# Kernel optimization log

Measured on AMD Instinct MI355X. Metric: run time of the kernel, lower is better.

## Reference

```python
import jax, jax.numpy as jnp
import numpy as np

D = 50          # half-window
K = 2 * D + 1   # 101 window positions
P_SIZE = 100    # predictive-alignment hidden dim


def setup_inputs() -> dict:
    key = jax.random.key(0)
    ks = jax.random.split(key, 5)
    B, S, CQ, CC = 2, 2048, 256, 256
    q = jax.random.normal(ks[0], (B, S, CQ), jnp.float32)
    c_t = jax.random.normal(ks[1], (B, S, CC), jnp.float32)
    W_a = jax.random.normal(ks[2], (CC, CQ), jnp.float32) / np.sqrt(CQ).astype(np.float32)
    W_p = jax.random.normal(ks[3], (P_SIZE, CC), jnp.float32) / np.sqrt(CC).astype(np.float32)
    V_p = jax.random.normal(ks[4], (1, P_SIZE), jnp.float32) / np.sqrt(P_SIZE).astype(np.float32)
    return {"q": q, "c_t": c_t, "W_a": W_a, "W_p": W_p, "V_p": V_p}


def reference(q, c_t, W_a, W_p, V_p):
    B, S, CQ = q.shape
    # predictive alignment: p in (0, S), one predicted center per (b, s)
    p = S * jax.nn.sigmoid(jnp.tanh(c_t @ W_p.T) @ V_p.T)[..., 0]          # [B,S]
    offs = jnp.arange(-D, D + 1)                                           # [K]
    # torch .long() truncates toward zero (raw can be negative)
    raw = jnp.trunc(p[..., None] + offs[None, None, :] + 1.0).astype(jnp.int32)
    # clamp to [0, S+1] then mod (S+1): index 0 == padded (invalid) row,
    # matching torch's NaN-padded row 0 (S+1 wraps to 0 via the modulo)
    idx = jnp.clip(raw, 0, S + 1) % (S + 1)                                # [B,S,K]
    mask = idx == 0                                                        # invalid window slots
    # pad row 0 (torch pads with NaN then zeroes the NaN rows; we pad with 0
    # and mask by index -> identical math for finite q)
    q_pad = jnp.concatenate([jnp.zeros((B, 1, CQ), q.dtype), q], axis=1)   # [B,S+1,CQ]
    gathered = jnp.take_along_axis(q_pad, idx.reshape(B, S * K, 1), axis=1)
    q1 = jnp.where(mask[..., None], 0.0, gathered.reshape(B, S, K, CQ))    # [B,S,K,CQ]
    # score: W_a projection then dot with context
    Wq = jnp.einsum("bskq,cq->bskc", q1, W_a)                              # [B,S,K,CC]
    a = jnp.einsum("bskc,bsc->bsk", Wq, c_t)                               # [B,S,K]
    a = jnp.where(mask, -jnp.inf, a)
    attn = jax.nn.softmax(a, axis=2)                                       # [B,S,K]
    # gaussian decay centered at floor(p) (p > 0 so trunc == floor)
    exponent = -2.0 * (((offs[None, None, :] + jnp.trunc(p)[..., None] - p[..., None]) / D) ** 2)
    w = attn * jnp.exp(exponent)                                           # [B,S,K]
    s_t = jnp.einsum("bsk,bskc->bsc", w, q1)                               # [B,S,CQ]
    return s_t
```

## Files before the change

### kernel.cpp

```cpp
#include <hip/hip_runtime.h>
#include <math.h>

#define S_LEN 2048
#define NB    2
#define CQ_   256
#define CC_   256
#define DH    50
#define KW    101
#define PS    100
#define RB    4
#define HPAD  128
#define WTH   1e-5f

__global__ __launch_bounds__(128) void k_prep(const float* __restrict__ Wp,
                                              float* __restrict__ WpT) {
  const int c = blockIdx.x, j = threadIdx.x;
  WpT[c * HPAD + j] = (j < PS) ? Wp[j * CC_ + c] : 0.0f;
}

__global__ __launch_bounds__(384, 6) void k_align(const float* __restrict__ ct,
    const float* __restrict__ Wa, const float* __restrict__ WpT,
    const float* __restrict__ Vp, float* __restrict__ p_out,
    float* __restrict__ V_out) {
  const int r0  = blockIdx.x * RB;
  const int tid = threadIdx.x;
  const float* crow = ct + (size_t)r0 * CC_;

  __shared__ float red[RB][PS + 4];

  if (tid < CQ_) {
    const float* wa = Wa + tid;
    float acc[RB];
#pragma unroll
    for (int r = 0; r < RB; ++r) acc[r] = 0.0f;

    float4 cv0[RB], cv1[RB];
#pragma unroll
    for (int r = 0; r < RB; ++r) cv0[r] = *(const float4*)&crow[r * CC_];
    float w00 = wa[0 * CQ_], w01 = wa[1 * CQ_], w02 = wa[2 * CQ_], w03 = wa[3 * CQ_];

    for (int c = 0; c < CC_ - 4; c += 4) {
      const int cn = c + 4;
#pragma unroll
      for (int r = 0; r < RB; ++r) cv1[r] = *(const float4*)&crow[r * CC_ + cn];
      const float w10 = wa[(size_t)(cn + 0) * CQ_];
      const float w11 = wa[(size_t)(cn + 1) * CQ_];
      const float w12 = wa[(size_t)(cn + 2) * CQ_];
      const float w13 = wa[(size_t)(cn + 3) * CQ_];
#pragma unroll
      for (int r = 0; r < RB; ++r) {
        float t = acc[r];
        t = fmaf(cv0[r].x, w00, t);
        t = fmaf(cv0[r].y, w01, t);
        t = fmaf(cv0[r].z, w02, t);
        t = fmaf(cv0[r].w, w03, t);
        acc[r] = t;
      }
#pragma unroll
      for (int r = 0; r < RB; ++r) cv0[r] = cv1[r];
      w00 = w10; w01 = w11; w02 = w12; w03 = w13;
    }
#pragma unroll
    for (int r = 0; r < RB; ++r) {
      float t = acc[r];
      t = fmaf(cv0[r].x, w00, t);
      t = fmaf(cv0[r].y, w01, t);
      t = fmaf(cv0[r].z, w02, t);
      t = fmaf(cv0[r].w, w03, t);
      acc[r] = t;
    }
#pragma unroll
    for (int r = 0; r < RB; ++r)
      V_out[(size_t)(r0 + r) * CQ_ + tid] = acc[r];
  } else {
    const int j = tid - CQ_;
    const float* wh = WpT + j;
    float ah[RB];
#pragma unroll
    for (int r = 0; r < RB; ++r) ah[r] = 0.0f;

    float4 cv0[RB], cv1[RB];
#pragma unroll
    for (int r = 0; r < RB; ++r) cv0[r] = *(const float4*)&crow[r * CC_];
    float w00 = wh[0 * HPAD], w01 = wh[1 * HPAD], w02 = wh[2 * HPAD], w03 = wh[3 * HPAD];

    for (int c = 0; c < CC_ - 4; c += 4) {
      const int cn = c + 4;
#pragma unroll
      for (int r = 0; r < RB; ++r) cv1[r] = *(const float4*)&crow[r * CC_ + cn];
      const float w10 = wh[(size_t)(cn + 0) * HPAD];
      const float w11 = wh[(size_t)(cn + 1) * HPAD];
      const float w12 = wh[(size_t)(cn + 2) * HPAD];
      const float w13 = wh[(size_t)(cn + 3) * HPAD];
#pragma unroll
      for (int r = 0; r < RB; ++r) {
        float t = ah[r];
        t = fmaf(cv0[r].x, w00, t);
        t = fmaf(cv0[r].y, w01, t);
        t = fmaf(cv0[r].z, w02, t);
        t = fmaf(cv0[r].w, w03, t);
        ah[r] = t;
      }
#pragma unroll
      for (int r = 0; r < RB; ++r) cv0[r] = cv1[r];
      w00 = w10; w01 = w11; w02 = w12; w03 = w13;
    }
#pragma unroll
    for (int r = 0; r < RB; ++r) {
      float t = ah[r];
      t = fmaf(cv0[r].x, w00, t);
      t = fmaf(cv0[r].y, w01, t);
      t = fmaf(cv0[r].z, w02, t);
      t = fmaf(cv0[r].w, w03, t);
      ah[r] = t;
    }
    if (j < PS) {
      const float vp = Vp[j];
#pragma unroll
      for (int r = 0; r < RB; ++r) red[r][j] = vp * tanhf(ah[r]);
    }
  }
  __syncthreads();
  if (tid < RB) {
    float s = 0.0f;
    for (int j = 0; j < PS; ++j) s += red[tid][j];
    p_out[r0 + tid] = (float)S_LEN * (1.0f / (1.0f + expf(-s)));
  }
}

__global__ __launch_bounds__(256, 8) void k_attn(const float* __restrict__ q,
    const float* __restrict__ p_in, const float* V,
    float* out) {
  const int tid  = threadIdx.x;
  const int wid  = tid >> 6;
  const int rloc = wid >> 1;
  const int half = wid & 1;
  const int row  = (blockIdx.x << 1) + rloc;
  const int lane = tid & 63;
  const int b    = row >> 11;

  __shared__ float ss[2][128];
  __shared__ float sw[2][128];
  __shared__ float sacc[4][CQ_];

  const float p  = p_in[row];
  const float tp = truncf(p);
  const float* qb = q + (size_t)b * S_LEN * CQ_;

  const int sub = lane >> 4;
  const int sl  = lane & 15;
  const int c4  = sl * 4;

  const float* vrow = V + (size_t)row * CQ_;
  const float4 v0 = *(const float4*)(vrow + c4);
  const float4 v1 = *(const float4*)(vrow + 64 + c4);
  const float4 v2 = *(const float4*)(vrow + 128 + c4);
  const float4 v3 = *(const float4*)(vrow + 192 + c4);

  if (lane >= KW - 64) ss[rloc][64 + lane] = -INFINITY;

  for (int gg = 0; gg < 13; gg += 2) {
    const int ga = half * 13 + gg;
    const int ka = (ga << 2) + sub;
    const int kb = ka + 4;
    const float ta = p + (float)(ka - DH) + 1.0f;
    const float tb = p + (float)(kb - DH) + 1.0f;
    const int rawa = (int)ta;
    const int rawb = (int)tb;
    const bool oka = (rawa >= 1) && (rawa <= S_LEN) && (ka < KW);
    const bool okb = (rawb >= 1) && (rawb <= S_LEN) && (kb < KW);
    const float* qra = qb + (size_t)(oka ? rawa - 1 : 0) * CQ_;
    const float* qrb = qb + (size_t)(okb ? rawb - 1 : 0) * CQ_;

    const float4 a0 = *(const float4*)(qra + c4);
    const float4 a1 = *(const float4*)(qra + 64 + c4);
    const float4 a2 = *(const float4*)(qra + 128 + c4);
    const float4 a3 = *(const float4*)(qra + 192 + c4);
    const float4 b0 = *(const float4*)(qrb + c4);
    const float4 b1 = *(const float4*)(qrb + 64 + c4);
    const float4 b2 = *(const float4*)(qrb + 128 + c4);
    const float4 b3 = *(const float4*)(qrb + 192 + c4);

    float t0 = a0.x * v0.x, t1 = a1.x * v1.x, t2 = a2.x * v2.x, t3 = a3.x * v3.x;
    t0 = fmaf(a0.y, v0.y, t0); t1 = fmaf(a1.y, v1.y, t1);
    t2 = fmaf(a2.y, v2.y, t2); t3 = fmaf(a3.y, v3.y, t3);
    t0 = fmaf(a0.z, v0.z, t0); t1 = fmaf(a1.z, v1.z, t1);
    t2 = fmaf(a2.z, v2.z, t2); t3 = fmaf(a3.z, v3.z, t3);
    t0 = fmaf(a0.w, v0.w, t0); t1 = fmaf(a1.w, v1.w, t1);
    t2 = fmaf(a2.w, v2.w, t2); t3 = fmaf(a3.w, v3.w, t3);
    float sA = (t0 + t1) + (t2 + t3);
    sA += __shfl_xor(sA, 1, 64);
    sA += __shfl_xor(sA, 2, 64);
    sA += __shfl_xor(sA, 4, 64);
    sA += __shfl_xor(sA, 8, 64);
    sA = oka ? sA : -INFINITY;
    if (sl == 0 && ka < 128) ss[rloc][ka] = sA;

    float u0 = b0.x * v0.x, u1 = b1.x * v1.x, u2 = b2.x * v2.x, u3 = b3.x * v3.x;
    u0 = fmaf(b0.y, v0.y, u0); u1 = fmaf(b1.y, v1.y, u1);
    u2 = fmaf(b2.y, v2.y, u2); u3 = fmaf(b3.y, v3.y, u3);
    u0 = fmaf(b0.z, v0.z, u0); u1 = fmaf(b1.z, v1.z, u1);
    u2 = fmaf(b2.z, v2.z, u2); u3 = fmaf(b3.z, v3.z, u3);
    u0 = fmaf(b0.w, v0.w, u0); u1 = fmaf(b1.w, v1.w, u1);
    u2 = fmaf(b2.w, v2.w, u2); u3 = fmaf(b3.w, v3.w, u3);
    float sB = (u0 + u1) + (u2 + u3);
    sB += __shfl_xor(sB, 1, 64);
    sB += __shfl_xor(sB, 2, 64);
    sB += __shfl_xor(sB, 4, 64);
    sB += __shfl_xor(sB, 8, 64);
    sB = okb ? sB : -INFINITY;
    if (sl == 0 && kb < 128) ss[rloc][kb] = sB;
  }
  __syncthreads();

  const float s0 = ss[rloc][lane];
  const float s1 = ss[rloc][64 + lane];

  float m = fmaxf(s0, s1);
#pragma unroll
  for (int off = 1; off < 64; off <<= 1) m = fmaxf(m, __shfl_xor(m, off, 64));

  const float e0 = __expf(s0 - m);
  const float e1 = __expf(s1 - m);
  float den = e0 + e1;
#pragma unroll
  for (int off = 1; off < 64; off <<= 1) den += __shfl_xor(den, off, 64);
  const float inv = 1.0f / den;

  float g0 = ((float)(lane - DH) + tp - p) / (float)DH;
  float g1 = ((float)(lane + (64 - DH)) + tp - p) / (float)DH;
  const float w0 = e0 * __expf(-2.0f * g0 * g0) * inv;
  const float w1 = e1 * __expf(-2.0f * g1 * g1) * inv;
  sw[rloc][lane] = w0;
  if (lane < KW - 64) sw[rloc][64 + lane] = w1;

  unsigned long long m0 = __ballot(w0 > WTH);
  unsigned long long m1 = __ballot((lane < KW - 64) && (w1 > WTH));

  float4 acc = make_float4(0.0f, 0.0f, 0.0f, 0.0f);
  int cnt = 0;
  while ((m0 | m1) != 0ull) {
    int kk[4];
#pragma unroll
    for (int i = 0; i < 4; ++i) {
      int k = -1;
      if (m0)      { k = __builtin_ctzll(m0);      m0 &= m0 - 1; }
      else if (m1) { k = 64 + __builtin_ctzll(m1); m1 &= m1 - 1; }
      kk[i] = k;
    }
#pragma unroll
    for (int i = 0; i < 4; ++i) {
      if (kk[i] >= 0) {
        if ((cnt & 1) == half) {
          const float wk = sw[rloc][kk[i]];
          const float t = p + (float)(kk[i] - DH) + 1.0f;
          const int r = (int)t - 1;
          const float4 qv = *(const float4*)(qb + (size_t)r * CQ_ + lane * 4);
          acc.x = fmaf(wk, qv.x, acc.x);
          acc.y = fmaf(wk, qv.y, acc.y);
          acc.z = fmaf(wk, qv.z, acc.z);
          acc.w = fmaf(wk, qv.w, acc.w);
        }
        ++cnt;
      }
    }
  }
  *(float4*)&sacc[wid][lane * 4] = acc;
  __syncthreads();

  const int row0 = (blockIdx.x << 1);
  out[(size_t)row0 * CQ_ + tid]       = sacc[0][tid] + sacc[1][tid];
  out[(size_t)(row0 + 1) * CQ_ + tid] = sacc[2][tid] + sacc[3][tid];
}

extern "C" void kernel_launch(void* const* d_in, const int* in_sizes, int n_in,
                              void* d_out, int out_size, void* d_ws, size_t ws_size,
                              hipStream_t stream) {
  const float* q  = (const float*)d_in[0];
  const float* ct = (const float*)d_in[1];
  const float* Wa = (const float*)d_in[2];
  const float* Wp = (const float*)d_in[3];
  const float* Vp = (const float*)d_in[4];
  float* out = (float*)d_out;

  float* ws     = (float*)d_ws;
  float* p_ws   = ws;
  float* WpT_ws = ws + NB * S_LEN;

  k_prep <<<CC_, HPAD, 0, stream>>>(Wp, WpT_ws);
  k_align<<<(NB * S_LEN) / RB, 384, 0, stream>>>(ct, Wa, WpT_ws, Vp, p_ws, out);
  k_attn <<<(NB * S_LEN) / 2, 256, 0, stream>>>(q, p_ws, out, out);
}
```

Before: 111.4 us.

## Fuse alignment projection and windowed attention into a single kernel

```diff
diff --git a/kernel.cpp b/kernel.cpp
--- a/kernel.cpp
+++ b/kernel.cpp
@@ -18,15 +18,20 @@
   WpT[c * HPAD + j] = (j < PS) ? Wp[j * CC_ + c] : 0.0f;
 }
 
-__global__ __launch_bounds__(384, 6) void k_align(const float* __restrict__ ct,
-    const float* __restrict__ Wa, const float* __restrict__ WpT,
-    const float* __restrict__ Vp, float* __restrict__ p_out,
-    float* __restrict__ V_out) {
+__global__ __launch_bounds__(512, 4) void k_fused(const float* __restrict__ q,
+    const float* __restrict__ ct, const float* __restrict__ Wa,
+    const float* __restrict__ WpT, const float* __restrict__ Vp,
+    float* __restrict__ out) {
   const int r0  = blockIdx.x * RB;
   const int tid = threadIdx.x;
   const float* crow = ct + (size_t)r0 * CC_;
 
+  __shared__ __align__(16) float sV[RB][CQ_];
   __shared__ float red[RB][PS + 4];
+  __shared__ float sp[RB];
+  __shared__ float ss[RB][128];
+  __shared__ float sw[RB][128];
+  __shared__ __align__(16) float sacc[8][CQ_];
 
   if (tid < CQ_) {
     const float* wa = Wa + tid;
@@ -70,9 +75,8 @@
       acc[r] = t;
     }
 #pragma unroll
-    for (int r = 0; r < RB; ++r)
-      V_out[(size_t)(r0 + r) * CQ_ + tid] = acc[r];
-  } else {
+    for (int r = 0; r < RB; ++r) sV[r][tid] = acc[r];
+  } else if (tid < CQ_ + PS) {
     const int j = tid - CQ_;
     const float* wh = WpT + j;
     float ah[RB];
@@ -114,36 +118,26 @@
       t = fmaf(cv0[r].w, w03, t);
       ah[r] = t;
     }
-    if (j < PS) {
-      const float vp = Vp[j];
-#pragma unroll
-      for (int r = 0; r < RB; ++r) red[r][j] = vp * tanhf(ah[r]);
-    }
+    const float vp = Vp[j];
+#pragma unroll
+    for (int r = 0; r < RB; ++r) red[r][j] = vp * tanhf(ah[r]);
   }
   __syncthreads();
   if (tid < RB) {
     float s = 0.0f;
     for (int j = 0; j < PS; ++j) s += red[tid][j];
-    p_out[r0 + tid] = (float)S_LEN * (1.0f / (1.0f + expf(-s)));
-  }
-}
-
-__global__ __launch_bounds__(256, 8) void k_attn(const float* __restrict__ q,
-    const float* __restrict__ p_in, const float* V,
-    float* out) {
-  const int tid  = threadIdx.x;
+    sp[tid] = (float)S_LEN * (1.0f / (1.0f + expf(-s)));
+  }
+  __syncthreads();
+
   const int wid  = tid >> 6;
   const int rloc = wid >> 1;
   const int half = wid & 1;
-  const int row  = (blockIdx.x << 1) + rloc;
+  const int row  = r0 + rloc;
   const int lane = tid & 63;
   const int b    = row >> 11;
 
-  __shared__ float ss[2][128];
-  __shared__ float sw[2][128];
-  __shared__ float sacc[4][CQ_];
-
-  const float p  = p_in[row];
+  const float p  = sp[rloc];
   const float tp = truncf(p);
   const float* qb = q + (size_t)b * S_LEN * CQ_;
 
@@ -151,11 +145,10 @@
   const int sl  = lane & 15;
   const int c4  = sl * 4;
 
-  const float* vrow = V + (size_t)row * CQ_;
-  const float4 v0 = *(const float4*)(vrow + c4);
-  const float4 v1 = *(const float4*)(vrow + 64 + c4);
-  const float4 v2 = *(const float4*)(vrow + 128 + c4);
-  const float4 v3 = *(const float4*)(vrow + 192 + c4);
+  const float4 v0 = *(const float4*)&sV[rloc][c4];
+  const float4 v1 = *(const float4*)&sV[rloc][64 + c4];
+  const float4 v2 = *(const float4*)&sV[rloc][128 + c4];
+  const float4 v3 = *(const float4*)&sV[rloc][192 + c4];
 
   if (lane >= KW - 64) ss[rloc][64 + lane] = -INFINITY;
 
@@ -268,9 +261,10 @@
   *(float4*)&sacc[wid][lane * 4] = acc;
   __syncthreads();
 
-  const int row0 = (blockIdx.x << 1);
-  out[(size_t)row0 * CQ_ + tid]       = sacc[0][tid] + sacc[1][tid];
-  out[(size_t)(row0 + 1) * CQ_ + tid] = sacc[2][tid] + sacc[3][tid];
+  const int rr = tid >> 8;
+  const int cc = tid & 255;
+  out[(size_t)(r0 + rr) * CQ_ + cc]     = sacc[2 * rr][cc]     + sacc[2 * rr + 1][cc];
+  out[(size_t)(r0 + rr + 2) * CQ_ + cc] = sacc[2 * rr + 4][cc] + sacc[2 * rr + 5][cc];
 }
 
 extern "C" void kernel_launch(void* const* d_in, const int* in_sizes, int n_in,
@@ -283,11 +277,8 @@
   const float* Vp = (const float*)d_in[4];
   float* out = (float*)d_out;
 
-  float* ws     = (float*)d_ws;
-  float* p_ws   = ws;
-  float* WpT_ws = ws + NB * S_LEN;
+  float* WpT_ws = (float*)d_ws;
 
   k_prep <<<CC_, HPAD, 0, stream>>>(Wp, WpT_ws);
-  k_align<<<(NB * S_LEN) / RB, 384, 0, stream>>>(ct, Wa, WpT_ws, Vp, p_ws, out);
-  k_attn <<<(NB * S_LEN) / 2, 256, 0, stream>>>(q, p_ws, out, out);
+  k_fused<<<(NB * S_LEN) / RB, 512, 0, stream>>>(q, ct, Wa, WpT_ws, Vp, out);
 }
```

After: 117.3 us. 5.3% more time.
